# Performance work log

Measured on AMD Instinct MI355X. Metric: run time of the kernel, lower is better.

The kernel has to match this reference:

```python
import jax, jax.numpy as jnp
import numpy as np

BN_EPS = 1e-5
EPS = 1e-12
ALPHA = 0.1
ITERS = 3

def _bn(x, gamma, beta, axes):
    # BatchNorm with batch stats (track_running_stats=False), biased variance
    mean = x.mean(axis=axes, keepdims=True)
    var = x.var(axis=axes, keepdims=True)
    return (x - mean) * jax.lax.rsqrt(var + BN_EPS) * gamma + beta

def setup_inputs() -> dict:
    key = jax.random.key(0)
    ks = jax.random.split(key, 4)
    b, c, h, w = 64, 512, 64, 64
    n = 32  # embed_num
    x = jax.random.normal(ks[0], (b, c, h, w), dtype=jnp.float32)
    meta_embed = jax.random.normal(ks[1], (n, c), dtype=jnp.float32)
    Wq = jax.random.normal(ks[2], (c, c), dtype=jnp.float32) * (1.0 / np.sqrt(c))
    bq = jax.random.normal(ks[3], (c,), dtype=jnp.float32) * 0.01
    return {
        "x": x, "meta_embed": meta_embed, "Wq": Wq, "bq": bq,
        "g1": jnp.ones((c,), jnp.float32), "b1": jnp.zeros((c,), jnp.float32),
        "g2": jnp.ones((n,), jnp.float32), "b2": jnp.zeros((n,), jnp.float32),
    }

def reference(x, meta_embed, Wq, bq, g1, b1, g2, b2):
    b, c, h, w = x.shape
    d = c
    inputs = x.reshape(b, c, h * w).transpose(0, 2, 1)  # (b, hw, d)
    k = inputs
    v = inputs
    n = meta_embed.shape[0]
    slots = jnp.broadcast_to(meta_embed[None], (b, n, d))
    new_slots = None
    for _ in range(ITERS):
        if new_slots is not None:
            slots = new_slots * ALPHA + slots * (1.0 - ALPHA)
        # to_q: Linear -> BatchNorm1d over flattened (b*n, d) -> ReLU
        q = slots.reshape(b * n, d) @ Wq.T + bq
        q = jax.nn.relu(_bn(q, g1, b1, axes=0)).reshape(b, n, d)
        attn = jnp.einsum('bid,bjd->bij', q, k)  # (b, n, hw)
        # mask_norm: BatchNorm1d over channels=n (reduce batch & hw) -> ReLU
        attn = jax.nn.relu(_bn(attn, g2[None, :, None], b2[None, :, None], axes=(0, 2)))
        new_slots = jnp.einsum('bjd,bij->bid', v, attn) / (attn.sum(-1, keepdims=True) + EPS)
    return new_slots
```

## Files before the change

kernel.cpp:

```cpp
#include <hip/hip_runtime.h>


#define F4(p)  (*reinterpret_cast<float4*>(p))
#define CF4(p) (*reinterpret_cast<const float4*>(p))

#define O_SUM1 0
#define O_SQ1  512
#define O_SUM2 1024
#define O_SQ2  1056
#define O_SC1  1088
#define O_SH1  1600
#define O_SC2  2112
#define O_SH2  2144
#define O_RS   2176

typedef __attribute__((address_space(1))) const void gvoid_t;
typedef __attribute__((address_space(3))) void lvoid_t;
__device__ __forceinline__ void gload_lds16(const float* g, float* l) {
    __builtin_amdgcn_global_load_lds((gvoid_t*)g, (lvoid_t*)l, 16, 0, 0);
}

__global__ __launch_bounds__(256) void k_transpose64(const float* __restrict__ A,
                                                     float* __restrict__ AT,
                                                     int R, int C) {
    __shared__ __align__(16) float tile[64][68];
    const int cb = blockIdx.x * 64;
    const int rb = blockIdx.y * 64;
    const size_t bofs = (size_t)blockIdx.z * R * C;
    const float* Ab = A + bofs;
    float* ATb = AT + bofs;
    const int t = threadIdx.x;
    const int g = t >> 4, h = t & 15;
    float4 v0 = CF4(Ab + (size_t)(rb + g * 4 + 0) * C + cb + h * 4);
    float4 v1 = CF4(Ab + (size_t)(rb + g * 4 + 1) * C + cb + h * 4);
    float4 v2 = CF4(Ab + (size_t)(rb + g * 4 + 2) * C + cb + h * 4);
    float4 v3 = CF4(Ab + (size_t)(rb + g * 4 + 3) * C + cb + h * 4);
    float4 w0 = {v0.x, v1.x, v2.x, v3.x};
    float4 w1 = {v0.y, v1.y, v2.y, v3.y};
    float4 w2 = {v0.z, v1.z, v2.z, v3.z};
    float4 w3 = {v0.w, v1.w, v2.w, v3.w};
    F4(&tile[h * 4 + 0][g * 4]) = w0;
    F4(&tile[h * 4 + 1][g * 4]) = w1;
    F4(&tile[h * 4 + 2][g * 4]) = w2;
    F4(&tile[h * 4 + 3][g * 4]) = w3;
    __syncthreads();
#pragma unroll
    for (int s = 0; s < 4; ++s) {
        int crow = g + 16 * s;
        F4(ATb + (size_t)(cb + crow) * R + rb + h * 4) = F4(&tile[crow][h * 4]);
    }
}

__global__ void k_init_slots(const float* __restrict__ meta, float* __restrict__ slots) {
    int f = blockIdx.x * 256 + threadIdx.x;
    int m = f >> 7;
    int d4 = f & 127;
    F4(slots + (size_t)f * 4) = CF4(meta + ((size_t)((m & 31) << 7) + d4) * 4);
}

__global__ void k_blend(float* __restrict__ slots, const float* __restrict__ ns) {
    int f = blockIdx.x * 256 + threadIdx.x;
    float4 s = F4(slots + (size_t)f * 4);
    float4 n = CF4(ns + (size_t)f * 4);
    s.x = 0.9f * s.x + 0.1f * n.x;
    s.y = 0.9f * s.y + 0.1f * n.y;
    s.z = 0.9f * s.z + 0.1f * n.z;
    s.w = 0.9f * s.w + 0.1f * n.w;
    F4(slots + (size_t)f * 4) = s;
}

__global__ void k_qinit(const float* __restrict__ bq, float* __restrict__ Q) {
    int f = blockIdx.x * 256 + threadIdx.x;
    F4(Q + (size_t)f * 4) = CF4(bq + (size_t)(f & 127) * 4);
}

__global__ void k_zero_out(float* __restrict__ out) {
    int f = blockIdx.x * 256 + threadIdx.x;
    float4 z = {0.f, 0.f, 0.f, 0.f};
    F4(out + (size_t)f * 4) = z;
}

__global__ __launch_bounds__(256) void k_qgemm(const float* __restrict__ S,
                                               const float* __restrict__ WqT,
                                               float* __restrict__ Q) {
    __shared__ __align__(16) float asT[32][36];
    __shared__ __align__(16) float bs[32][512];
    const int m0 = blockIdx.x * 32;
    const int kbase = blockIdx.y * 128;
    const int t = threadIdx.x;
    const int w = t >> 6, l = t & 63;
    const int ty = w, tx = l;
    float c[8][8] = {};
    for (int ch = 0; ch < 4; ++ch) {
        int k0 = kbase + ch * 32;
        {
            int m = t >> 3, kq = t & 7;
            float4 v = CF4(S + (size_t)(m0 + m) * 512 + k0 + kq * 4);
            asT[kq * 4 + 0][m] = v.x; asT[kq * 4 + 1][m] = v.y;
            asT[kq * 4 + 2][m] = v.z; asT[kq * 4 + 3][m] = v.w;
        }
#pragma unroll
        for (int cc = 0; cc < 16; ++cc) {
            int chunk = w * 16 + cc;
            int row = chunk >> 1, half = chunk & 1;
            const float* src = WqT + (size_t)(k0 + row) * 512 + half * 256 + l * 4;
            gload_lds16(src, &bs[row][half * 256]);
        }
        __syncthreads();
#pragma unroll 8
        for (int k = 0; k < 32; ++k) {
            float4 a0 = F4(&asT[k][ty * 8]);
            float4 a1 = F4(&asT[k][ty * 8 + 4]);
            float4 b0 = F4(&bs[k][tx * 4]);
            float4 b1 = F4(&bs[k][256 + tx * 4]);
            float av[8] = {a0.x, a0.y, a0.z, a0.w, a1.x, a1.y, a1.z, a1.w};
            float bv[8] = {b0.x, b0.y, b0.z, b0.w, b1.x, b1.y, b1.z, b1.w};
#pragma unroll
            for (int ii = 0; ii < 8; ++ii)
#pragma unroll
                for (int jj = 0; jj < 8; ++jj)
                    c[ii][jj] = fmaf(av[ii], bv[jj], c[ii][jj]);
        }
        __syncthreads();
    }
#pragma unroll
    for (int ii = 0; ii < 8; ++ii) {
        float* dst = Q + (size_t)(m0 + ty * 8 + ii) * 512;
#pragma unroll
        for (int q = 0; q < 4; ++q) atomicAdd(dst + tx * 4 + q, c[ii][q]);
#pragma unroll
        for (int q = 0; q < 4; ++q) atomicAdd(dst + 256 + tx * 4 + q, c[ii][4 + q]);
    }
}

__global__ void k_zero_stats(float* __restrict__ stats) {
    int i = blockIdx.x * 256 + threadIdx.x;
    if (i < 1088) stats[i] = 0.0f;
}

__global__ __launch_bounds__(256) void k_bn1_stats(const float* __restrict__ Q,
                                                   float* __restrict__ stats) {
    int cg = blockIdx.x & 7, rc = blockIdx.x >> 3;
    int lc = threadIdx.x & 63;
    int col = cg * 64 + lc;
    int rsub = threadIdx.x >> 6;
    float s = 0.f, sq = 0.f;
    for (int k = 0; k < 64; ++k) {
        float v = Q[(size_t)(rc * 256 + rsub + 4 * k) * 512 + col];
        s += v;
        sq += v * v;
    }
    __shared__ float ls[4][64], lq[4][64];
    ls[rsub][lc] = s;
    lq[rsub][lc] = sq;
    __syncthreads();
    if (threadIdx.x < 64) {
        int tcol = threadIdx.x;
        float ts = ls[0][tcol] + ls[1][tcol] + ls[2][tcol] + ls[3][tcol];
        float tq = lq[0][tcol] + lq[1][tcol] + lq[2][tcol] + lq[3][tcol];
        atomicAdd(&stats[O_SUM1 + cg * 64 + tcol], ts);
        atomicAdd(&stats[O_SQ1 + cg * 64 + tcol], tq);
    }
}

__global__ void k_bn1_fin(float* __restrict__ stats, const float* __restrict__ g1,
                          const float* __restrict__ b1) {
    int c = threadIdx.x;
    float mean = stats[O_SUM1 + c] * (1.0f / 2048.0f);
    float var = stats[O_SQ1 + c] * (1.0f / 2048.0f) - mean * mean;
    float sc = rsqrtf(var + 1e-5f) * g1[c];
    stats[O_SC1 + c] = sc;
    stats[O_SH1 + c] = b1[c] - mean * sc;
}

__global__ void k_bn1_apply(float* __restrict__ Q, const float* __restrict__ stats) {
    int f = blockIdx.x * 256 + threadIdx.x;
    int col4 = f & 127;
    float4 v = F4(Q + (size_t)f * 4);
    float4 sc = CF4(stats + O_SC1 + col4 * 4);
    float4 sh = CF4(stats + O_SH1 + col4 * 4);
    v.x = fmaxf(fmaf(v.x, sc.x, sh.x), 0.f);
    v.y = fmaxf(fmaf(v.y, sc.y, sh.y), 0.f);
    v.z = fmaxf(fmaf(v.z, sc.z, sh.z), 0.f);
    v.w = fmaxf(fmaf(v.w, sc.w, sh.w), 0.f);
    F4(Q + (size_t)f * 4) = v;
}

__global__ __launch_bounds__(256) void k_gemm1(const float* __restrict__ Q,
                                               const float* __restrict__ X,
                                               float* __restrict__ attn) {
    __shared__ __align__(16) float qsT[32][36];
    __shared__ __align__(16) float xs[32][512];
    const int b = blockIdx.y;
    const int j0 = blockIdx.x * 512;
    const int t = threadIdx.x;
    const int w = t >> 6, l = t & 63;
    const int ty = w, tx = l;
    const float* qb = Q + (size_t)b * 32 * 512;
    const float* xb = X + (size_t)b * 512 * 4096 + j0;
    float c[8][8] = {};
    for (int k0 = 0; k0 < 512; k0 += 32) {
        {
            int i = t >> 3, kq = t & 7;
            float4 v = CF4(qb + (size_t)i * 512 + k0 + kq * 4);
            qsT[kq * 4 + 0][i] = v.x; qsT[kq * 4 + 1][i] = v.y;
            qsT[kq * 4 + 2][i] = v.z; qsT[kq * 4 + 3][i] = v.w;
        }
#pragma unroll
        for (int cc = 0; cc < 16; ++cc) {
            int chunk = w * 16 + cc;
            int row = chunk >> 1, half = chunk & 1;
            const float* src = xb + (size_t)(k0 + row) * 4096 + half * 256 + l * 4;
            gload_lds16(src, &xs[row][half * 256]);
        }
        __syncthreads();
#pragma unroll 8
        for (int k = 0; k < 32; ++k) {
            float4 a0 = F4(&qsT[k][ty * 8]);
            float4 a1 = F4(&qsT[k][ty * 8 + 4]);
            float4 b0 = F4(&xs[k][tx * 4]);
            float4 b1 = F4(&xs[k][256 + tx * 4]);
            float av[8] = {a0.x, a0.y, a0.z, a0.w, a1.x, a1.y, a1.z, a1.w};
            float bv[8] = {b0.x, b0.y, b0.z, b0.w, b1.x, b1.y, b1.z, b1.w};
#pragma unroll
            for (int ii = 0; ii < 8; ++ii)
#pragma unroll
                for (int jj = 0; jj < 8; ++jj)
                    c[ii][jj] = fmaf(av[ii], bv[jj], c[ii][jj]);
        }
        __syncthreads();
    }
#pragma unroll
    for (int ii = 0; ii < 8; ++ii) {
        float* dst = attn + (size_t)(b * 32 + ty * 8 + ii) * 4096 + j0;
        float4 r0 = {c[ii][0], c[ii][1], c[ii][2], c[ii][3]};
        float4 r1 = {c[ii][4], c[ii][5], c[ii][6], c[ii][7]};
        F4(dst + tx * 4) = r0;
        F4(dst + 256 + tx * 4) = r1;
    }
}

__global__ __launch_bounds__(256) void k_bn2_stats(const float* __restrict__ attn,
                                                   float* __restrict__ stats) {
    int i = blockIdx.x, b = blockIdx.y;
    const float* p = attn + (size_t)(b * 32 + i) * 4096;
    int t = threadIdx.x;
    float s = 0.f, sq = 0.f;
#pragma unroll
    for (int c = 0; c < 4; ++c) {
        float4 v = CF4(p + (size_t)(t + 256 * c) * 4);
        s += v.x + v.y + v.z + v.w;
        sq += v.x * v.x + v.y * v.y + v.z * v.z + v.w * v.w;
    }
    __shared__ float rs[256], rq[256];
    rs[t] = s; rq[t] = sq;
    __syncthreads();
    for (int off = 128; off > 0; off >>= 1) {
        if (t < off) { rs[t] += rs[t + off]; rq[t] += rq[t + off]; }
        __syncthreads();
    }
    if (t == 0) {
        atomicAdd(&stats[O_SUM2 + i], rs[0]);
        atomicAdd(&stats[O_SQ2 + i], rq[0]);
    }
}

__global__ void k_bn2_fin(float* __restrict__ stats, const float* __restrict__ g2,
                          const float* __restrict__ b2) {
    int i = threadIdx.x;
    const float inv = 1.0f / 262144.0f;
    float mean = stats[O_SUM2 + i] * inv;
    float var = stats[O_SQ2 + i] * inv - mean * mean;
    float sc = rsqrtf(var + 1e-5f) * g2[i];
    stats[O_SC2 + i] = sc;
    stats[O_SH2 + i] = b2[i] - mean * sc;
}

__global__ __launch_bounds__(256) void k_bn2_apply(float* __restrict__ attn,
                                                   float* __restrict__ stats) {
    int i = blockIdx.x, b = blockIdx.y;
    float* p = attn + (size_t)(b * 32 + i) * 4096;
    float sc = stats[O_SC2 + i], sh = stats[O_SH2 + i];
    int t = threadIdx.x;
    float s = 0.f;
#pragma unroll
    for (int c = 0; c < 4; ++c) {
        float4 v = F4(p + (size_t)(t + 256 * c) * 4);
        v.x = fmaxf(fmaf(v.x, sc, sh), 0.f);
        v.y = fmaxf(fmaf(v.y, sc, sh), 0.f);
        v.z = fmaxf(fmaf(v.z, sc, sh), 0.f);
        v.w = fmaxf(fmaf(v.w, sc, sh), 0.f);
        s += v.x + v.y + v.z + v.w;
        F4(p + (size_t)(t + 256 * c) * 4) = v;
    }
    __shared__ float rs[256];
    rs[t] = s;
    __syncthreads();
    for (int off = 128; off > 0; off >>= 1) {
        if (t < off) rs[t] += rs[t + off];
        __syncthreads();
    }
    if (t == 0) stats[O_RS + b * 32 + i] = rs[0];
}

__global__ __launch_bounds__(256) void k_gemm2(const float* __restrict__ attn,
                                               const float* __restrict__ XT,
                                               const float* __restrict__ stats,
                                               float* __restrict__ out) {
    __shared__ __align__(16) float asT[32][36];
    __shared__ __align__(16) float xs[32][512];
    const int b = blockIdx.y;
    const int jbase0 = blockIdx.x * 512;
    const int t = threadIdx.x;
    const int w = t >> 6, l = t & 63;
    const int ty = w, tx = l;
    const float* ab = attn + (size_t)b * 32 * 4096 + jbase0;
    const float* xb = XT + (size_t)b * 4096 * 512 + (size_t)jbase0 * 512;
    float c[8][8] = {};
    for (int ch = 0; ch < 16; ++ch) {
        int jb = ch * 32;
        {
            int i = t >> 3, jq = t & 7;
            float4 v = CF4(ab + (size_t)i * 4096 + jb + jq * 4);
            asT[jq * 4 + 0][i] = v.x; asT[jq * 4 + 1][i] = v.y;
            asT[jq * 4 + 2][i] = v.z; asT[jq * 4 + 3][i] = v.w;
        }
#pragma unroll
        for (int cc = 0; cc < 16; ++cc) {
            int chunk = w * 16 + cc;
            int row = chunk >> 1, half = chunk & 1;
            const float* src = xb + (size_t)(jb + row) * 512 + half * 256 + l * 4;
            gload_lds16(src, &xs[row][half * 256]);
        }
        __syncthreads();
#pragma unroll 8
        for (int k = 0; k < 32; ++k) {
            float4 a0 = F4(&asT[k][ty * 8]);
            float4 a1 = F4(&asT[k][ty * 8 + 4]);
            float4 b0 = F4(&xs[k][tx * 4]);
            float4 b1 = F4(&xs[k][256 + tx * 4]);
            float av[8] = {a0.x, a0.y, a0.z, a0.w, a1.x, a1.y, a1.z, a1.w};
            float bv[8] = {b0.x, b0.y, b0.z, b0.w, b1.x, b1.y, b1.z, b1.w};
#pragma unroll
            for (int ii = 0; ii < 8; ++ii)
#pragma unroll
                for (int jj = 0; jj < 8; ++jj)
                    c[ii][jj] = fmaf(av[ii], bv[jj], c[ii][jj]);
        }
        __syncthreads();
    }
#pragma unroll
    for (int ii = 0; ii < 8; ++ii) {
        int row = b * 32 + ty * 8 + ii;
        float inv = 1.0f / (stats[O_RS + row] + 1e-12f);
        float* dst = out + (size_t)row * 512;
#pragma unroll
        for (int q = 0; q < 4; ++q) atomicAdd(dst + tx * 4 + q, c[ii][q] * inv);
#pragma unroll
        for (int q = 0; q < 4; ++q) atomicAdd(dst + 256 + tx * 4 + q, c[ii][4 + q] * inv);
    }
}

extern "C" void kernel_launch(void* const* d_in, const int* in_sizes, int n_in,
                              void* d_out, int out_size, void* d_ws, size_t ws_size,
                              hipStream_t stream) {
    const float* x    = (const float*)d_in[0];
    const float* meta = (const float*)d_in[1];
    const float* Wq   = (const float*)d_in[2];
    const float* bq   = (const float*)d_in[3];
    const float* g1   = (const float*)d_in[4];
    const float* b1   = (const float*)d_in[5];
    const float* g2   = (const float*)d_in[6];
    const float* b2   = (const float*)d_in[7];
    float* out = (float*)d_out;

    float* ws = (float*)d_ws;
    float* slots = ws;
    float* q     = ws + 1048576;
    float* attn  = ws + 2097152;
    float* stats = ws + 10485760;
    float* wqT   = ws + 10489984;
    float* xT    = ws + 16777216;

    k_transpose64<<<dim3(8, 8, 1), 256, 0, stream>>>(Wq, wqT, 512, 512);
    k_transpose64<<<dim3(64, 8, 64), 256, 0, stream>>>(x, xT, 512, 4096);

    k_init_slots<<<1024, 256, 0, stream>>>(meta, slots);
    for (int it = 0; it < 3; ++it) {
        if (it > 0) k_blend<<<1024, 256, 0, stream>>>(slots, out);
        k_qinit<<<1024, 256, 0, stream>>>(bq, q);
        k_qgemm<<<dim3(64, 4), 256, 0, stream>>>(slots, wqT, q);
        k_zero_stats<<<5, 256, 0, stream>>>(stats);
        k_bn1_stats<<<64, 256, 0, stream>>>(q, stats);
        k_bn1_fin<<<1, 512, 0, stream>>>(stats, g1, b1);
        k_bn1_apply<<<1024, 256, 0, stream>>>(q, stats);
        k_gemm1<<<dim3(8, 64), 256, 0, stream>>>(q, x, attn);
        k_bn2_stats<<<dim3(32, 64), 256, 0, stream>>>(attn, stats);
        k_bn2_fin<<<1, 32, 0, stream>>>(stats, g2, b2);
        k_bn2_apply<<<dim3(32, 64), 256, 0, stream>>>(attn, stats);
        k_zero_out<<<1024, 256, 0, stream>>>(out);
        k_gemm2<<<dim3(8, 64), 256, 0, stream>>>(attn, xT, stats, out);
    }
}
```

Measured before the change: 2.306 ms.

## Fuse BatchNorm stats and apply into GEMMs with double-buffered LDS pipelines

BN1 statistics move into the Q GEMM epilogue, which now also adds the bias and writes Q directly with no atomics. The BN1 apply moves into the gemm1 operand load, BN2 statistics into the gemm1 epilogue, and the BN2 apply plus row sums into the gemm2 operand load. All three GEMMs get double-buffered LDS prefetch. gemm2 writes split-K partials to a buffer reduced by a new finalize kernel instead of atomically accumulating into a zeroed output. This removes several full passes over the large attention tensor and many launches, at the cost of more LDS per block and an extra partial buffer.

```diff
diff --git a/kernel.cpp b/kernel.cpp
--- a/kernel.cpp
+++ b/kernel.cpp
@@ -69,97 +69,86 @@
     F4(slots + (size_t)f * 4) = s;
 }
 
-__global__ void k_qinit(const float* __restrict__ bq, float* __restrict__ Q) {
-    int f = blockIdx.x * 256 + threadIdx.x;
-    F4(Q + (size_t)f * 4) = CF4(bq + (size_t)(f & 127) * 4);
-}
-
-__global__ void k_zero_out(float* __restrict__ out) {
-    int f = blockIdx.x * 256 + threadIdx.x;
-    float4 z = {0.f, 0.f, 0.f, 0.f};
-    F4(out + (size_t)f * 4) = z;
+__global__ void k_zero_stats(float* __restrict__ stats) {
+    int i = threadIdx.x;
+#pragma unroll
+    for (int s = 0; s < 4; ++s) stats[i + 256 * s] = 0.0f;
 }
 
 __global__ __launch_bounds__(256) void k_qgemm(const float* __restrict__ S,
                                                const float* __restrict__ WqT,
-                                               float* __restrict__ Q) {
-    __shared__ __align__(16) float asT[32][36];
-    __shared__ __align__(16) float bs[32][512];
-    const int m0 = blockIdx.x * 32;
-    const int kbase = blockIdx.y * 128;
+                                               const float* __restrict__ bq,
+                                               float* __restrict__ Q,
+                                               float* __restrict__ stats) {
+    __shared__ __align__(16) float asT[512][16];
+    __shared__ __align__(16) float bs[2][32][256];
+    __shared__ __align__(16) float ls[4][256], lq[4][256];
+    const int m0 = blockIdx.x * 16;
+    const int n0 = blockIdx.y * 256;
     const int t = threadIdx.x;
     const int w = t >> 6, l = t & 63;
     const int ty = w, tx = l;
-    float c[8][8] = {};
-    for (int ch = 0; ch < 4; ++ch) {
-        int k0 = kbase + ch * 32;
-        {
-            int m = t >> 3, kq = t & 7;
-            float4 v = CF4(S + (size_t)(m0 + m) * 512 + k0 + kq * 4);
-            asT[kq * 4 + 0][m] = v.x; asT[kq * 4 + 1][m] = v.y;
-            asT[kq * 4 + 2][m] = v.z; asT[kq * 4 + 3][m] = v.w;
-        }
-#pragma unroll
-        for (int cc = 0; cc < 16; ++cc) {
-            int chunk = w * 16 + cc;
-            int row = chunk >> 1, half = chunk & 1;
-            const float* src = WqT + (size_t)(k0 + row) * 512 + half * 256 + l * 4;
-            gload_lds16(src, &bs[row][half * 256]);
-        }
-        __syncthreads();
+    {
+        int m = t & 15, fq = t >> 4;
+#pragma unroll
+        for (int s = 0; s < 8; ++s) {
+            int k = fq * 4 + s * 64;
+            float4 v = CF4(S + (size_t)(m0 + m) * 512 + k);
+            asT[k + 0][m] = v.x; asT[k + 1][m] = v.y;
+            asT[k + 2][m] = v.z; asT[k + 3][m] = v.w;
+        }
+    }
+#pragma unroll
+    for (int cc = 0; cc < 8; ++cc) {
+        int r = w * 8 + cc;
+        gload_lds16(WqT + (size_t)r * 512 + n0 + l * 4, &bs[0][r][0]);
+    }
+    __syncthreads();
+    float c[4][4] = {};
+    int cur = 0;
+    for (int tgl = 0; tgl < 16; ++tgl) {
+        if (tgl < 15) {
+            int k1 = (tgl + 1) * 32;
+#pragma unroll
+            for (int cc = 0; cc < 8; ++cc) {
+                int r = w * 8 + cc;
+                gload_lds16(WqT + (size_t)(k1 + r) * 512 + n0 + l * 4, &bs[cur ^ 1][r][0]);
+            }
+        }
+        int k0 = tgl * 32;
 #pragma unroll 8
         for (int k = 0; k < 32; ++k) {
-            float4 a0 = F4(&asT[k][ty * 8]);
-            float4 a1 = F4(&asT[k][ty * 8 + 4]);
-            float4 b0 = F4(&bs[k][tx * 4]);
-            float4 b1 = F4(&bs[k][256 + tx * 4]);
-            float av[8] = {a0.x, a0.y, a0.z, a0.w, a1.x, a1.y, a1.z, a1.w};
-            float bv[8] = {b0.x, b0.y, b0.z, b0.w, b1.x, b1.y, b1.z, b1.w};
-#pragma unroll
-            for (int ii = 0; ii < 8; ++ii)
-#pragma unroll
-                for (int jj = 0; jj < 8; ++jj)
+            float4 a = F4(&asT[k0 + k][ty * 4]);
+            float4 b = F4(&bs[cur][k][tx * 4]);
+            float av[4] = {a.x, a.y, a.z, a.w};
+            float bv[4] = {b.x, b.y, b.z, b.w};
+#pragma unroll
+            for (int ii = 0; ii < 4; ++ii)
+#pragma unroll
+                for (int jj = 0; jj < 4; ++jj)
                     c[ii][jj] = fmaf(av[ii], bv[jj], c[ii][jj]);
         }
         __syncthreads();
-    }
-#pragma unroll
-    for (int ii = 0; ii < 8; ++ii) {
-        float* dst = Q + (size_t)(m0 + ty * 8 + ii) * 512;
-#pragma unroll
-        for (int q = 0; q < 4; ++q) atomicAdd(dst + tx * 4 + q, c[ii][q]);
-#pragma unroll
-        for (int q = 0; q < 4; ++q) atomicAdd(dst + 256 + tx * 4 + q, c[ii][4 + q]);
-    }
-}
-
-__global__ void k_zero_stats(float* __restrict__ stats) {
-    int i = blockIdx.x * 256 + threadIdx.x;
-    if (i < 1088) stats[i] = 0.0f;
-}
-
-__global__ __launch_bounds__(256) void k_bn1_stats(const float* __restrict__ Q,
-                                                   float* __restrict__ stats) {
-    int cg = blockIdx.x & 7, rc = blockIdx.x >> 3;
-    int lc = threadIdx.x & 63;
-    int col = cg * 64 + lc;
-    int rsub = threadIdx.x >> 6;
-    float s = 0.f, sq = 0.f;
-    for (int k = 0; k < 64; ++k) {
-        float v = Q[(size_t)(rc * 256 + rsub + 4 * k) * 512 + col];
-        s += v;
-        sq += v * v;
-    }
-    __shared__ float ls[4][64], lq[4][64];
-    ls[rsub][lc] = s;
-    lq[rsub][lc] = sq;
+        cur ^= 1;
+    }
+    float4 bias = CF4(bq + n0 + tx * 4);
+    float4 sv = {0.f, 0.f, 0.f, 0.f}, qv = {0.f, 0.f, 0.f, 0.f};
+#pragma unroll
+    for (int ii = 0; ii < 4; ++ii) {
+        float4 v = {c[ii][0] + bias.x, c[ii][1] + bias.y,
+                    c[ii][2] + bias.z, c[ii][3] + bias.w};
+        F4(Q + (size_t)(m0 + ty * 4 + ii) * 512 + n0 + tx * 4) = v;
+        sv.x += v.x; sv.y += v.y; sv.z += v.z; sv.w += v.w;
+        qv.x += v.x * v.x; qv.y += v.y * v.y; qv.z += v.z * v.z; qv.w += v.w * v.w;
+    }
+    F4(&ls[ty][tx * 4]) = sv;
+    F4(&lq[ty][tx * 4]) = qv;
     __syncthreads();
-    if (threadIdx.x < 64) {
-        int tcol = threadIdx.x;
-        float ts = ls[0][tcol] + ls[1][tcol] + ls[2][tcol] + ls[3][tcol];
-        float tq = lq[0][tcol] + lq[1][tcol] + lq[2][tcol] + lq[3][tcol];
-        atomicAdd(&stats[O_SUM1 + cg * 64 + tcol], ts);
-        atomicAdd(&stats[O_SQ1 + cg * 64 + tcol], tq);
+    {
+        float s  = ls[0][t] + ls[1][t] + ls[2][t] + ls[3][t];
+        float q2 = lq[0][t] + lq[1][t] + lq[2][t] + lq[3][t];
+        atomicAdd(&stats[O_SUM1 + n0 + t], s);
+        atomicAdd(&stats[O_SQ1 + n0 + t], q2);
     }
 }
 
@@ -171,26 +160,15 @@
     float sc = rsqrtf(var + 1e-5f) * g1[c];
     stats[O_SC1 + c] = sc;
     stats[O_SH1 + c] = b1[c] - mean * sc;
-}
-
-__global__ void k_bn1_apply(float* __restrict__ Q, const float* __restrict__ stats) {
-    int f = blockIdx.x * 256 + threadIdx.x;
-    int col4 = f & 127;
-    float4 v = F4(Q + (size_t)f * 4);
-    float4 sc = CF4(stats + O_SC1 + col4 * 4);
-    float4 sh = CF4(stats + O_SH1 + col4 * 4);
-    v.x = fmaxf(fmaf(v.x, sc.x, sh.x), 0.f);
-    v.y = fmaxf(fmaf(v.y, sc.y, sh.y), 0.f);
-    v.z = fmaxf(fmaf(v.z, sc.z, sh.z), 0.f);
-    v.w = fmaxf(fmaf(v.w, sc.w, sh.w), 0.f);
-    F4(Q + (size_t)f * 4) = v;
+    if (c < 64) stats[O_SUM2 + c] = 0.0f;
 }
 
 __global__ __launch_bounds__(256) void k_gemm1(const float* __restrict__ Q,
                                                const float* __restrict__ X,
+                                               float* __restrict__ stats,
                                                float* __restrict__ attn) {
-    __shared__ __align__(16) float qsT[32][36];
-    __shared__ __align__(16) float xs[32][512];
+    __shared__ __align__(16) float qsT[2][32][36];
+    __shared__ __align__(16) float xs[2][32][512];
     const int b = blockIdx.y;
     const int j0 = blockIdx.x * 512;
     const int t = threadIdx.x;
@@ -198,28 +176,50 @@
     const int ty = w, tx = l;
     const float* qb = Q + (size_t)b * 32 * 512;
     const float* xb = X + (size_t)b * 512 * 4096 + j0;
-    float c[8][8] = {};
-    for (int k0 = 0; k0 < 512; k0 += 32) {
-        {
-            int i = t >> 3, kq = t & 7;
-            float4 v = CF4(qb + (size_t)i * 512 + k0 + kq * 4);
-            qsT[kq * 4 + 0][i] = v.x; qsT[kq * 4 + 1][i] = v.y;
-            qsT[kq * 4 + 2][i] = v.z; qsT[kq * 4 + 3][i] = v.w;
-        }
+    const int ai = t >> 3, akq = t & 7;
+    {
 #pragma unroll
         for (int cc = 0; cc < 16; ++cc) {
             int chunk = w * 16 + cc;
             int row = chunk >> 1, half = chunk & 1;
-            const float* src = xb + (size_t)(k0 + row) * 4096 + half * 256 + l * 4;
-            gload_lds16(src, &xs[row][half * 256]);
-        }
-        __syncthreads();
+            gload_lds16(xb + (size_t)row * 4096 + half * 256 + l * 4,
+                        &xs[0][row][half * 256]);
+        }
+        float4 v = CF4(qb + (size_t)ai * 512 + akq * 4);
+        float4 sc = CF4(stats + O_SC1 + akq * 4);
+        float4 sh = CF4(stats + O_SH1 + akq * 4);
+        v.x = fmaxf(fmaf(v.x, sc.x, sh.x), 0.f);
+        v.y = fmaxf(fmaf(v.y, sc.y, sh.y), 0.f);
+        v.z = fmaxf(fmaf(v.z, sc.z, sh.z), 0.f);
+        v.w = fmaxf(fmaf(v.w, sc.w, sh.w), 0.f);
+        qsT[0][akq * 4 + 0][ai] = v.x; qsT[0][akq * 4 + 1][ai] = v.y;
+        qsT[0][akq * 4 + 2][ai] = v.z; qsT[0][akq * 4 + 3][ai] = v.w;
+    }
+    __syncthreads();
+    float c[8][8] = {};
+    int cur = 0;
+    for (int tgl = 0; tgl < 16; ++tgl) {
+        float4 va, vsc, vsh;
+        const bool pf = tgl < 15;
+        if (pf) {
+            int k1 = (tgl + 1) * 32;
+#pragma unroll
+            for (int cc = 0; cc < 16; ++cc) {
+                int chunk = w * 16 + cc;
+                int row = chunk >> 1, half = chunk & 1;
+                gload_lds16(xb + (size_t)(k1 + row) * 4096 + half * 256 + l * 4,
+                            &xs[cur ^ 1][row][half * 256]);
+            }
+            va  = CF4(qb + (size_t)ai * 512 + k1 + akq * 4);
+            vsc = CF4(stats + O_SC1 + k1 + akq * 4);
+            vsh = CF4(stats + O_SH1 + k1 + akq * 4);
+        }
 #pragma unroll 8
         for (int k = 0; k < 32; ++k) {
-            float4 a0 = F4(&qsT[k][ty * 8]);
-            float4 a1 = F4(&qsT[k][ty * 8 + 4]);
-            float4 b0 = F4(&xs[k][tx * 4]);
-            float4 b1 = F4(&xs[k][256 + tx * 4]);
+            float4 a0 = F4(&qsT[cur][k][ty * 8]);
+            float4 a1 = F4(&qsT[cur][k][ty * 8 + 4]);
+            float4 b0 = F4(&xs[cur][k][tx * 4]);
+            float4 b1 = F4(&xs[cur][k][256 + tx * 4]);
             float av[8] = {a0.x, a0.y, a0.z, a0.w, a1.x, a1.y, a1.z, a1.w};
             float bv[8] = {b0.x, b0.y, b0.z, b0.w, b1.x, b1.y, b1.z, b1.w};
 #pragma unroll
@@ -228,7 +228,18 @@
                 for (int jj = 0; jj < 8; ++jj)
                     c[ii][jj] = fmaf(av[ii], bv[jj], c[ii][jj]);
         }
+        if (pf) {
+            va.x = fmaxf(fmaf(va.x, vsc.x, vsh.x), 0.f);
+            va.y = fmaxf(fmaf(va.y, vsc.y, vsh.y), 0.f);
+            va.z = fmaxf(fmaf(va.z, vsc.z, vsh.z), 0.f);
+            va.w = fmaxf(fmaf(va.w, vsc.w, vsh.w), 0.f);
+            qsT[cur ^ 1][akq * 4 + 0][ai] = va.x;
+            qsT[cur ^ 1][akq * 4 + 1][ai] = va.y;
+            qsT[cur ^ 1][akq * 4 + 2][ai] = va.z;
+            qsT[cur ^ 1][akq * 4 + 3][ai] = va.w;
+        }
         __syncthreads();
+        cur ^= 1;
     }
 #pragma unroll
     for (int ii = 0; ii < 8; ++ii) {
@@ -237,108 +248,94 @@
         float4 r1 = {c[ii][4], c[ii][5], c[ii][6], c[ii][7]};
         F4(dst + tx * 4) = r0;
         F4(dst + 256 + tx * 4) = r1;
-    }
-}
-
-__global__ __launch_bounds__(256) void k_bn2_stats(const float* __restrict__ attn,
-                                                   float* __restrict__ stats) {
-    int i = blockIdx.x, b = blockIdx.y;
-    const float* p = attn + (size_t)(b * 32 + i) * 4096;
-    int t = threadIdx.x;
-    float s = 0.f, sq = 0.f;
-#pragma unroll
-    for (int c = 0; c < 4; ++c) {
-        float4 v = CF4(p + (size_t)(t + 256 * c) * 4);
-        s += v.x + v.y + v.z + v.w;
-        sq += v.x * v.x + v.y * v.y + v.z * v.z + v.w * v.w;
-    }
-    __shared__ float rs[256], rq[256];
-    rs[t] = s; rq[t] = sq;
-    __syncthreads();
-    for (int off = 128; off > 0; off >>= 1) {
-        if (t < off) { rs[t] += rs[t + off]; rq[t] += rq[t + off]; }
-        __syncthreads();
-    }
-    if (t == 0) {
-        atomicAdd(&stats[O_SUM2 + i], rs[0]);
-        atomicAdd(&stats[O_SQ2 + i], rq[0]);
+        float s  = r0.x + r0.y + r0.z + r0.w + r1.x + r1.y + r1.z + r1.w;
+        float q2 = r0.x * r0.x + r0.y * r0.y + r0.z * r0.z + r0.w * r0.w +
+                   r1.x * r1.x + r1.y * r1.y + r1.z * r1.z + r1.w * r1.w;
+#pragma unroll
+        for (int off = 32; off > 0; off >>= 1) {
+            s  += __shfl_down(s, off, 64);
+            q2 += __shfl_down(q2, off, 64);
+        }
+        if (tx == 0) {
+            atomicAdd(&stats[O_SUM2 + ty * 8 + ii], s);
+            atomicAdd(&stats[O_SQ2 + ty * 8 + ii], q2);
+        }
     }
 }
 
 __global__ void k_bn2_fin(float* __restrict__ stats, const float* __restrict__ g2,
                           const float* __restrict__ b2) {
-    int i = threadIdx.x;
-    const float inv = 1.0f / 262144.0f;
-    float mean = stats[O_SUM2 + i] * inv;
-    float var = stats[O_SQ2 + i] * inv - mean * mean;
-    float sc = rsqrtf(var + 1e-5f) * g2[i];
-    stats[O_SC2 + i] = sc;
-    stats[O_SH2 + i] = b2[i] - mean * sc;
-}
-
-__global__ __launch_bounds__(256) void k_bn2_apply(float* __restrict__ attn,
-                                                   float* __restrict__ stats) {
-    int i = blockIdx.x, b = blockIdx.y;
-    float* p = attn + (size_t)(b * 32 + i) * 4096;
-    float sc = stats[O_SC2 + i], sh = stats[O_SH2 + i];
     int t = threadIdx.x;
-    float s = 0.f;
-#pragma unroll
-    for (int c = 0; c < 4; ++c) {
-        float4 v = F4(p + (size_t)(t + 256 * c) * 4);
-        v.x = fmaxf(fmaf(v.x, sc, sh), 0.f);
-        v.y = fmaxf(fmaf(v.y, sc, sh), 0.f);
-        v.z = fmaxf(fmaf(v.z, sc, sh), 0.f);
-        v.w = fmaxf(fmaf(v.w, sc, sh), 0.f);
-        s += v.x + v.y + v.z + v.w;
-        F4(p + (size_t)(t + 256 * c) * 4) = v;
-    }
-    __shared__ float rs[256];
-    rs[t] = s;
-    __syncthreads();
-    for (int off = 128; off > 0; off >>= 1) {
-        if (t < off) rs[t] += rs[t + off];
-        __syncthreads();
-    }
-    if (t == 0) stats[O_RS + b * 32 + i] = rs[0];
+    if (t < 32) {
+        const float inv = 1.0f / 262144.0f;
+        float mean = stats[O_SUM2 + t] * inv;
+        float var = stats[O_SQ2 + t] * inv - mean * mean;
+        float sc = rsqrtf(var + 1e-5f) * g2[t];
+        stats[O_SC2 + t] = sc;
+        stats[O_SH2 + t] = b2[t] - mean * sc;
+    }
+#pragma unroll
+    for (int s = 0; s < 8; ++s) stats[O_RS + t + 256 * s] = 0.0f;
 }
 
 __global__ __launch_bounds__(256) void k_gemm2(const float* __restrict__ attn,
                                                const float* __restrict__ XT,
-                                               const float* __restrict__ stats,
-                                               float* __restrict__ out) {
-    __shared__ __align__(16) float asT[32][36];
-    __shared__ __align__(16) float xs[32][512];
+                                               float* __restrict__ stats,
+                                               float* __restrict__ part) {
+    __shared__ __align__(16) float asT[2][32][36];
+    __shared__ __align__(16) float xs[2][32][512];
     const int b = blockIdx.y;
-    const int jbase0 = blockIdx.x * 512;
+    const int sp = blockIdx.x;
+    const int jbase0 = sp * 1024;
     const int t = threadIdx.x;
     const int w = t >> 6, l = t & 63;
     const int ty = w, tx = l;
     const float* ab = attn + (size_t)b * 32 * 4096 + jbase0;
     const float* xb = XT + (size_t)b * 4096 * 512 + (size_t)jbase0 * 512;
-    float c[8][8] = {};
-    for (int ch = 0; ch < 16; ++ch) {
-        int jb = ch * 32;
-        {
-            int i = t >> 3, jq = t & 7;
-            float4 v = CF4(ab + (size_t)i * 4096 + jb + jq * 4);
-            asT[jq * 4 + 0][i] = v.x; asT[jq * 4 + 1][i] = v.y;
-            asT[jq * 4 + 2][i] = v.z; asT[jq * 4 + 3][i] = v.w;
-        }
+    const int ai = t >> 3, ajq = t & 7;
+    const float scA = stats[O_SC2 + ai];
+    const float shA = stats[O_SH2 + ai];
+    float rsum = 0.f;
+    {
 #pragma unroll
         for (int cc = 0; cc < 16; ++cc) {
             int chunk = w * 16 + cc;
             int row = chunk >> 1, half = chunk & 1;
-            const float* src = xb + (size_t)(jb + row) * 512 + half * 256 + l * 4;
-            gload_lds16(src, &xs[row][half * 256]);
-        }
-        __syncthreads();
+            gload_lds16(xb + (size_t)row * 512 + half * 256 + l * 4,
+                        &xs[0][row][half * 256]);
+        }
+        float4 v = CF4(ab + (size_t)ai * 4096 + ajq * 4);
+        v.x = fmaxf(fmaf(v.x, scA, shA), 0.f);
+        v.y = fmaxf(fmaf(v.y, scA, shA), 0.f);
+        v.z = fmaxf(fmaf(v.z, scA, shA), 0.f);
+        v.w = fmaxf(fmaf(v.w, scA, shA), 0.f);
+        rsum += v.x + v.y + v.z + v.w;
+        asT[0][ajq * 4 + 0][ai] = v.x; asT[0][ajq * 4 + 1][ai] = v.y;
+        asT[0][ajq * 4 + 2][ai] = v.z; asT[0][ajq * 4 + 3][ai] = v.w;
+    }
+    __syncthreads();
+    float c[8][8] = {};
+    int cur = 0;
+    for (int tgl = 0; tgl < 32; ++tgl) {
+        float4 va;
+        const bool pf = tgl < 31;
+        if (pf) {
+            int jb = (tgl + 1) * 32;
+#pragma unroll
+            for (int cc = 0; cc < 16; ++cc) {
+                int chunk = w * 16 + cc;
+                int row = chunk >> 1, half = chunk & 1;
+                gload_lds16(xb + (size_t)(jb + row) * 512 + half * 256 + l * 4,
+                            &xs[cur ^ 1][row][half * 256]);
+            }
+            va = CF4(ab + (size_t)ai * 4096 + jb + ajq * 4);
+        }
 #pragma unroll 8
         for (int k = 0; k < 32; ++k) {
-            float4 a0 = F4(&asT[k][ty * 8]);
-            float4 a1 = F4(&asT[k][ty * 8 + 4]);
-            float4 b0 = F4(&xs[k][tx * 4]);
-            float4 b1 = F4(&xs[k][256 + tx * 4]);
+            float4 a0 = F4(&asT[cur][k][ty * 8]);
+            float4 a1 = F4(&asT[cur][k][ty * 8 + 4]);
+            float4 b0 = F4(&xs[cur][k][tx * 4]);
+            float4 b1 = F4(&xs[cur][k][256 + tx * 4]);
             float av[8] = {a0.x, a0.y, a0.z, a0.w, a1.x, a1.y, a1.z, a1.w};
             float bv[8] = {b0.x, b0.y, b0.z, b0.w, b1.x, b1.y, b1.z, b1.w};
 #pragma unroll
@@ -347,18 +344,48 @@
                 for (int jj = 0; jj < 8; ++jj)
                     c[ii][jj] = fmaf(av[ii], bv[jj], c[ii][jj]);
         }
+        if (pf) {
+            va.x = fmaxf(fmaf(va.x, scA, shA), 0.f);
+            va.y = fmaxf(fmaf(va.y, scA, shA), 0.f);
+            va.z = fmaxf(fmaf(va.z, scA, shA), 0.f);
+            va.w = fmaxf(fmaf(va.w, scA, shA), 0.f);
+            rsum += va.x + va.y + va.z + va.w;
+            asT[cur ^ 1][ajq * 4 + 0][ai] = va.x;
+            asT[cur ^ 1][ajq * 4 + 1][ai] = va.y;
+            asT[cur ^ 1][ajq * 4 + 2][ai] = va.z;
+            asT[cur ^ 1][ajq * 4 + 3][ai] = va.w;
+        }
         __syncthreads();
-    }
+        cur ^= 1;
+    }
+    rsum += __shfl_down(rsum, 4, 8);
+    rsum += __shfl_down(rsum, 2, 8);
+    rsum += __shfl_down(rsum, 1, 8);
+    if ((t & 7) == 0) atomicAdd(&stats[O_RS + b * 32 + ai], rsum);
 #pragma unroll
     for (int ii = 0; ii < 8; ++ii) {
-        int row = b * 32 + ty * 8 + ii;
-        float inv = 1.0f / (stats[O_RS + row] + 1e-12f);
-        float* dst = out + (size_t)row * 512;
-#pragma unroll
-        for (int q = 0; q < 4; ++q) atomicAdd(dst + tx * 4 + q, c[ii][q] * inv);
-#pragma unroll
-        for (int q = 0; q < 4; ++q) atomicAdd(dst + 256 + tx * 4 + q, c[ii][4 + q] * inv);
-    }
+        float* dst = part + ((size_t)sp * 2048 + b * 32 + ty * 8 + ii) * 512;
+        float4 r0 = {c[ii][0], c[ii][1], c[ii][2], c[ii][3]};
+        float4 r1 = {c[ii][4], c[ii][5], c[ii][6], c[ii][7]};
+        F4(dst + tx * 4) = r0;
+        F4(dst + 256 + tx * 4) = r1;
+    }
+}
+
+__global__ void k_finout(const float* __restrict__ part, const float* __restrict__ stats,
+                         float* __restrict__ out) {
+    int f = blockIdx.x * 256 + threadIdx.x;
+    int row = f >> 7;
+    float4 v0 = CF4(part + (size_t)f * 4);
+    float4 v1 = CF4(part + 1048576 + (size_t)f * 4);
+    float4 v2 = CF4(part + 2097152 + (size_t)f * 4);
+    float4 v3 = CF4(part + 3145728 + (size_t)f * 4);
+    float inv = 1.0f / (stats[O_RS + row] + 1e-12f);
+    float4 o = {(v0.x + v1.x + v2.x + v3.x) * inv,
+                (v0.y + v1.y + v2.y + v3.y) * inv,
+                (v0.z + v1.z + v2.z + v3.z) * inv,
+                (v0.w + v1.w + v2.w + v3.w) * inv};
+    F4(out + (size_t)f * 4) = o;
 }
 
 extern "C" void kernel_launch(void* const* d_in, const int* in_sizes, int n_in,
@@ -379,7 +406,8 @@
     float* q     = ws + 1048576;
     float* attn  = ws + 2097152;
     float* stats = ws + 10485760;
-    float* wqT   = ws + 10489984;
+    float* part  = ws + 10489984;
+    float* wqT   = ws + 14684288;
     float* xT    = ws + 16777216;
 
     k_transpose64<<<dim3(8, 8, 1), 256, 0, stream>>>(Wq, wqT, 512, 512);
@@ -388,17 +416,12 @@
     k_init_slots<<<1024, 256, 0, stream>>>(meta, slots);
     for (int it = 0; it < 3; ++it) {
         if (it > 0) k_blend<<<1024, 256, 0, stream>>>(slots, out);
-        k_qinit<<<1024, 256, 0, stream>>>(bq, q);
-        k_qgemm<<<dim3(64, 4), 256, 0, stream>>>(slots, wqT, q);
-        k_zero_stats<<<5, 256, 0, stream>>>(stats);
-        k_bn1_stats<<<64, 256, 0, stream>>>(q, stats);
+        k_zero_stats<<<1, 256, 0, stream>>>(stats);
+        k_qgemm<<<dim3(128, 2), 256, 0, stream>>>(slots, wqT, bq, q, stats);
         k_bn1_fin<<<1, 512, 0, stream>>>(stats, g1, b1);
-        k_bn1_apply<<<1024, 256, 0, stream>>>(q, stats);
-        k_gemm1<<<dim3(8, 64), 256, 0, stream>>>(q, x, attn);
-        k_bn2_stats<<<dim3(32, 64), 256, 0, stream>>>(attn, stats);
-        k_bn2_fin<<<1, 32, 0, stream>>>(stats, g2, b2);
-        k_bn2_apply<<<dim3(32, 64), 256, 0, stream>>>(attn, stats);
-        k_zero_out<<<1024, 256, 0, stream>>>(out);
-        k_gemm2<<<dim3(8, 64), 256, 0, stream>>>(attn, xT, stats, out);
-    }
-}
+        k_gemm1<<<dim3(8, 64), 256, 0, stream>>>(q, x, stats, attn);
+        k_bn2_fin<<<1, 256, 0, stream>>>(stats, g2, b2);
+        k_gemm2<<<dim3(4, 64), 256, 0, stream>>>(attn, xT, stats, part);
+        k_finout<<<1024, 256, 0, stream>>>(part, stats, out);
+    }
+}
```

Result: slower. 2.368 ms (+2.7%).
